# Optimization experiments

Measured on AMD Instinct MI355X. Metric: run time of the kernel, lower is better.

The kernel has to match this reference:

```python
import jax, jax.numpy as jnp
import numpy as np

D_MODEL = 1024
N_HEADS = 16
D_HEAD = D_MODEL // N_HEADS
D_FF = 4096
BATCH = 2
SEQ = 2048
LN_EPS = 1e-5


def setup_inputs() -> dict:
    key = jax.random.key(0)
    ks = jax.random.split(key, 12)
    s = 1.0 / np.sqrt(D_MODEL)
    x = jax.random.normal(ks[0], (BATCH, SEQ, D_MODEL), dtype=jnp.float32)
    mask = jnp.broadcast_to(jnp.tril(jnp.ones((SEQ, SEQ), jnp.int32)), (BATCH, SEQ, SEQ))
    return {
        "x": x,
        "mask": mask,
        # per-head projections stacked: [H, D, Dh] (bias=False in source)
        "Wq": jax.random.normal(ks[1], (N_HEADS, D_MODEL, D_HEAD), jnp.float32) * s,
        "Wk": jax.random.normal(ks[2], (N_HEADS, D_MODEL, D_HEAD), jnp.float32) * s,
        "Wv": jax.random.normal(ks[3], (N_HEADS, D_MODEL, D_HEAD), jnp.float32) * s,
        "Wo": jax.random.normal(ks[4], (D_MODEL, D_MODEL), jnp.float32) * s,
        "ln1_w": jnp.ones((D_MODEL,), jnp.float32),
        "ln1_b": jnp.zeros((D_MODEL,), jnp.float32),
        "ln2_w": jnp.ones((D_MODEL,), jnp.float32),
        "ln2_b": jnp.zeros((D_MODEL,), jnp.float32),
        "W1": jax.random.normal(ks[5], (D_MODEL, D_FF), jnp.float32) * s,
        "b1": jnp.zeros((D_FF,), jnp.float32),
        "W2": jax.random.normal(ks[6], (D_FF, D_MODEL), jnp.float32) * (1.0 / np.sqrt(D_FF)),
        "b2": jnp.zeros((D_MODEL,), jnp.float32),
    }


def layer_norm(x, w, b):
    mu = jnp.mean(x, axis=-1, keepdims=True)
    var = jnp.var(x, axis=-1, keepdims=True)
    return (x - mu) * jax.lax.rsqrt(var + LN_EPS) * w + b


def reference(x, mask, Wq, Wk, Wv, Wo, ln1_w, ln1_b, ln2_w, ln2_b, W1, b1, W2, b2):
    # pre-LN masked self-attention
    h = layer_norm(x, ln1_w, ln1_b)
    q = jnp.einsum("bsd,hde->bhse", h, Wq)  # [B,H,S,Dh]
    k = jnp.einsum("bsd,hde->bhse", h, Wk)
    v = jnp.einsum("bsd,hde->bhse", h, Wv)
    scores = jnp.einsum("bhse,bhte->bhst", q, k) / np.sqrt(D_HEAD)
    scores = jnp.where(mask[:, None, :, :].astype(bool), scores, -jnp.inf)
    weights = jax.nn.softmax(scores, axis=-1)
    attn = jnp.einsum("bhst,bhte->bhse", weights, v)  # [B,H,S,Dh]
    # concat heads (head order = last-dim order in torch.cat)
    concat = attn.transpose(0, 2, 1, 3).reshape(x.shape[0], x.shape[1], D_MODEL)
    att_out = concat @ Wo
    att_x = x + att_out
    # FFN with exact (erf) GELU, matching nn.GELU default
    h2 = layer_norm(att_x, ln2_w, ln2_b)
    ff = jax.nn.gelu(h2 @ W1 + b1, approximate=False) @ W2 + b2
    return att_x + ff
```

## Files before the change

kernel.cpp:

```cpp
#include <hip/hip_runtime.h>
#include <hip/hip_bf16.h>
#include <math.h>

#define D_MODEL 1024
#define N_HEADS 16
#define D_HEAD  64
#define D_FF    4096
#define BATCH   2
#define SEQ     2048
#define NTOK    (BATCH*SEQ)

typedef __hip_bfloat16 bf16;
typedef __attribute__((ext_vector_type(8))) short short8;
typedef __attribute__((ext_vector_type(4))) float floatx4;

template<typename TIN>
__global__ void ln_kernel(const TIN* __restrict__ x,
                          const float* __restrict__ w,
                          const float* __restrict__ b,
                          bf16* __restrict__ out) {
    int row = blockIdx.x;
    int tid = threadIdx.x;
    const long base = (long)row * D_MODEL;
    float v[4];
    float s = 0.f, sq = 0.f;
#pragma unroll
    for (int i = 0; i < 4; ++i) {
        float xv = (float)x[base + tid + i*256];
        v[i] = xv; s += xv; sq += xv*xv;
    }
    __shared__ float r1[256], r2[256];
    r1[tid] = s; r2[tid] = sq; __syncthreads();
    for (int off = 128; off > 0; off >>= 1) {
        if (tid < off) { r1[tid] += r1[tid+off]; r2[tid] += r2[tid+off]; }
        __syncthreads();
    }
    float mean = r1[0] * (1.f/D_MODEL);
    float var  = r2[0] * (1.f/D_MODEL) - mean*mean;
    float rstd = rsqrtf(var + 1e-5f);
#pragma unroll
    for (int i = 0; i < 4; ++i) {
        int c = tid + i*256;
        out[base + c] = __float2bfloat16((v[i] - mean) * rstd * w[c] + b[c]);
    }
}

__global__ __launch_bounds__(256) void wcvt_kernel(const float* __restrict__ W,
                                                   bf16* __restrict__ Wt,
                                                   int K, int N) {
    __shared__ float t[32][33];
    int n0 = blockIdx.x * 32, k0 = blockIdx.y * 32;
    int lx = threadIdx.x & 31, ly = threadIdx.x >> 5;
#pragma unroll
    for (int i = 0; i < 4; ++i) {
        int k = ly + i * 8;
        t[k][lx] = W[(long)(k0 + k) * N + n0 + lx];
    }
    __syncthreads();
#pragma unroll
    for (int i = 0; i < 4; ++i) {
        int n = ly + i * 8;
        Wt[(long)(n0 + n) * K + k0 + lx] = __float2bfloat16(t[lx][n]);
    }
}

__global__ __launch_bounds__(256) void wcvt_wo_w1(const float* __restrict__ Wo,
                                                  const float* __restrict__ W1,
                                                  bf16* __restrict__ wo_bf,
                                                  bf16* __restrict__ w1_bf) {
    __shared__ float t[32][33];
    int gx = blockIdx.x;
    const float* W; bf16* Wt; int N, n0;
    if (gx < 32) { W = Wo; Wt = wo_bf; N = D_MODEL; n0 = gx * 32; }
    else         { W = W1; Wt = w1_bf; N = D_FF;    n0 = (gx - 32) * 32; }
    int k0 = blockIdx.y * 32;
    int lx = threadIdx.x & 31, ly = threadIdx.x >> 5;
#pragma unroll
    for (int i = 0; i < 4; ++i) {
        int k = ly + i * 8;
        t[k][lx] = W[(long)(k0 + k) * N + n0 + lx];
    }
    __syncthreads();
#pragma unroll
    for (int i = 0; i < 4; ++i) {
        int n = ly + i * 8;
        Wt[(long)(n0 + n) * D_MODEL + k0 + lx] = __float2bfloat16(t[lx][n]);
    }
}

__global__ __launch_bounds__(256) void wcvt_qkv(const float* __restrict__ Wq,
                                                const float* __restrict__ Wk,
                                                const float* __restrict__ Wv,
                                                bf16* __restrict__ outp) {
    __shared__ float t[32][33];
    int z = blockIdx.z, mat = z >> 4, head = z & 15;
    const float* W = (mat == 0 ? Wq : mat == 1 ? Wk : Wv) + (long)head * D_MODEL * D_HEAD;
    bf16* Wt = outp + (long)z * D_HEAD * D_MODEL;
    int n0 = blockIdx.x * 32, k0 = blockIdx.y * 32;
    int lx = threadIdx.x & 31, ly = threadIdx.x >> 5;
#pragma unroll
    for (int i = 0; i < 4; ++i) {
        int k = ly + i * 8;
        t[k][lx] = W[(long)(k0 + k) * D_HEAD + n0 + lx];
    }
    __syncthreads();
#pragma unroll
    for (int i = 0; i < 4; ++i) {
        int n = ly + i * 8;
        Wt[(long)(n0 + n) * D_MODEL + k0 + lx] = __float2bfloat16(t[lx][n]);
    }
}

__device__ inline void swz2d(int& bx, int& by) {
    int gx = gridDim.x;
    int nwg = gx * gridDim.y;
    int bid = blockIdx.y * gx + blockIdx.x;
    int swz = (bid & 7) * (nwg >> 3) + (bid >> 3);
    bx = swz % gx;
    by = swz / gx;
}

template<int ROWS>
__device__ inline void stage_tile(const bf16* g, int gstride, short* lds) {
    int lane = threadIdx.x & 63, wave = threadIdx.x >> 6;
#pragma unroll
    for (int it = 0; it < ROWS / 64; ++it) {
        int c = wave + it * 4;
        const bf16* gp = g + (long)(c * 16 + (lane >> 2)) * gstride + (lane & 3) * 8;
        short* lp = lds + c * 512 + lane * 8;
        __builtin_amdgcn_global_load_lds(
            (const __attribute__((address_space(1))) void*)gp,
            (__attribute__((address_space(3))) void*)lp, 16, 0, 0);
    }
}

template<int BM, int BN, int BK>
__device__ inline void gemm_accum(const bf16* __restrict__ A, int lda,
                                  const bf16* __restrict__ Wt, int K,
                                  int row0, int col0, short* As, short* Bs,
                                  floatx4 (&acc)[BM/32][BN/32]) {
    constexpr int MI  = BM / 32;
    constexpr int NR  = BN / 32;
    constexpr int ASZ = BM * BK;
    constexpr int BSZ = BN * BK;
    int tid  = threadIdx.x;
    int wave = tid >> 6, lane = tid & 63;
    int quad = lane >> 4, l16 = lane & 15;
    int wm = (wave >> 1) * (BM / 2);
    int wn = (wave & 1) * (BN / 2);

    auto stage = [&](int k0, int buf) {
#pragma unroll
        for (int kk = 0; kk < BK; kk += 32) {
            stage_tile<BM>(A  + (long)row0 * lda + k0 + kk, lda,
                           As + buf * ASZ + (kk / 32) * BM * 32);
            stage_tile<BN>(Wt + (long)col0 * K   + k0 + kk, K,
                           Bs + buf * BSZ + (kk / 32) * BN * 32);
        }
    };

    stage(0, 0);
    __syncthreads();

    int cur = 0;
    for (int k0 = 0; k0 < K; k0 += BK) {
        if (k0 + BK < K) stage(k0 + BK, cur ^ 1);

#pragma unroll
        for (int p = 0; p < BK / 32; ++p) {
            const short* Ap = As + cur * ASZ + p * BM * 32;
            const short* Bp = Bs + cur * BSZ + p * BN * 32;
            short8 af[MI], bfr[NR];
#pragma unroll
            for (int mi = 0; mi < MI; ++mi)
                af[mi] = *(const short8*)&Ap[(wm + mi * 16 + l16) * 32 + quad * 8];
#pragma unroll
            for (int ni = 0; ni < NR; ++ni)
                bfr[ni] = *(const short8*)&Bp[(wn + ni * 16 + l16) * 32 + quad * 8];
#pragma unroll
            for (int mi = 0; mi < MI; ++mi)
#pragma unroll
                for (int ni = 0; ni < NR; ++ni)
                    acc[mi][ni] = __builtin_amdgcn_mfma_f32_16x16x32_bf16(
                        af[mi], bfr[ni], acc[mi][ni], 0, 0, 0);
        }
        __syncthreads();
        cur ^= 1;
    }
}

template<int BM, int BN, int BK, int BIAS, int ACT, int RES, int OUTBF16>
__global__ __launch_bounds__(256) void mfma_gemm_bf(
    const bf16* __restrict__ A, int lda,
    const bf16* __restrict__ Wt, int K,
    const float* __restrict__ bias, const float* __restrict__ resid,
    void* __restrict__ Cout, int ldc)
{
    constexpr int MI = BM / 32;
    constexpr int NR = BN / 32;
    __shared__ short As[2 * BM * BK];
    __shared__ short Bs[2 * BN * BK];
    int bx, by; swz2d(bx, by);
    int row0 = by * BM, col0 = bx * BN;
    int tid = threadIdx.x, wave = tid >> 6, lane = tid & 63;
    int quad = lane >> 4, l16 = lane & 15;
    int wm = (wave >> 1) * (BM / 2);
    int wn = (wave & 1) * (BN / 2);

    floatx4 acc[MI][NR];
#pragma unroll
    for (int mi = 0; mi < MI; ++mi)
#pragma unroll
        for (int ni = 0; ni < NR; ++ni)
            acc[mi][ni] = (floatx4){0.f, 0.f, 0.f, 0.f};

    gemm_accum<BM, BN, BK>(A, lda, Wt, K, row0, col0, As, Bs, acc);

#pragma unroll
    for (int mi = 0; mi < MI; ++mi) {
#pragma unroll
        for (int ni = 0; ni < NR; ++ni) {
#pragma unroll
            for (int r = 0; r < 4; ++r) {
                int row = row0 + wm + mi * 16 + quad * 4 + r;
                int col = col0 + wn + ni * 16 + l16;
                float v = acc[mi][ni][r];
                if (BIAS) v += bias[col];
                if (ACT == 1) {
                    float x2 = v * v;
                    float arg = fminf(v * fmaf(0.1029392f, x2, 2.3021182f), 20.f);
                    float t = exp2f(arg);
                    v = v * t * __builtin_amdgcn_rcpf(t + 1.f);
                }
                long idx = (long)row * ldc + col;
                if (RES == 1) v += resid[idx];
                if (OUTBF16) ((bf16*)Cout)[idx] = __float2bfloat16(v);
                else         ((float*)Cout)[idx] = v;
            }
        }
    }
}

struct QkvOut { bf16* o[3]; };
__global__ __launch_bounds__(256) void qkv_kernel(const bf16* __restrict__ h1,
                                                  const bf16* __restrict__ wqkv,
                                                  QkvOut a) {
    __shared__ short As[2 * 128 * 32];
    __shared__ short Bs[2 * 128 * 32];
    int bx, by; swz2d(bx, by);
    int row0 = by * 128, col0 = bx * 128;
    int tid = threadIdx.x, wave = tid >> 6, lane = tid & 63;
    int quad = lane >> 4, l16 = lane & 15;
    int wm = (wave >> 1) * 64, wn = (wave & 1) * 64;

    floatx4 acc[4][4];
#pragma unroll
    for (int mi = 0; mi < 4; ++mi)
#pragma unroll
        for (int ni = 0; ni < 4; ++ni)
            acc[mi][ni] = (floatx4){0.f, 0.f, 0.f, 0.f};

    gemm_accum<128, 128, 32>(h1, D_MODEL, wqkv, D_MODEL, row0, col0, As, Bs, acc);

#pragma unroll
    for (int mi = 0; mi < 4; ++mi) {
#pragma unroll
        for (int ni = 0; ni < 4; ++ni) {
#pragma unroll
            for (int r = 0; r < 4; ++r) {
                int row = row0 + wm + mi * 16 + quad * 4 + r;
                int c   = col0 + wn + ni * 16 + l16;
                int mat = c >> 10, hd = (c >> 6) & 15, d = c & 63;
                int b = row >> 11, s = row & 2047;
                a.o[mat][(((long)(b * 16 + hd) * SEQ + s) << 6) + d] =
                    __float2bfloat16(acc[mi][ni][r]);
            }
        }
    }
}

__global__ __launch_bounds__(256) void fattn_mfma(const bf16* __restrict__ q,
                                                  const bf16* __restrict__ k,
                                                  const bf16* __restrict__ v,
                                                  bf16* __restrict__ po,
                                                  float* __restrict__ lz) {
    int byr = blockIdx.y;
    int tile = (byr < 8) ? byr : 23 - byr;
    int chunk = blockIdx.z;
    int bh = blockIdx.x;
    int tid = threadIdx.x;
    int wave = tid >> 6, lane = tid & 63;
    int quad = lane >> 4, l16 = lane & 15;
    const long base = (long)bh * SEQ * D_HEAD;
    const int r0g = tile * 128;

    bf16*  pob = po + (long)chunk * 32 * SEQ * 64;
    float* lzb = lz + (long)chunk * 32 * SEQ;

    __shared__ short Ks[64 * 72];
    __shared__ short Vt[64 * 72];
    __shared__ short Ps[4][32 * 72];

    short8 qf[2][2];
#pragma unroll
    for (int rb = 0; rb < 2; ++rb) {
        const short* qrow = (const short*)(q + base +
            (long)(r0g + wave * 32 + rb * 16 + l16) * D_HEAD);
        qf[rb][0] = *(const short8*)(qrow + quad * 8);
        qf[rb][1] = *(const short8*)(qrow + 32 + quad * 8);
#pragma unroll
        for (int c = 0; c < 2; ++c)
#pragma unroll
            for (int j = 0; j < 8; ++j) {
                float f = __uint_as_float(((unsigned)(unsigned short)qf[rb][c][j]) << 16)
                          * 0.18033688f;
                qf[rb][c][j] = __builtin_bit_cast(short, __float2bfloat16(f));
            }
    }

    short8 onesf;
    {
        short o1 = (l16 == 0) ? (short)0x3F80 : (short)0;
#pragma unroll
        for (int j = 0; j < 8; ++j) onesf[j] = o1;
    }

    floatx4 o[2][4];
#pragma unroll
    for (int rb = 0; rb < 2; ++rb)
#pragma unroll
        for (int nb = 0; nb < 4; ++nb) o[rb][nb] = (floatx4){0.f, 0.f, 0.f, 0.f};
    floatx4 l4[2] = {(floatx4){0.f,0.f,0.f,0.f}, (floatx4){0.f,0.f,0.f,0.f}};

    const int kt0 = chunk ? tile + 1 : 0;
    const int kt1 = chunk ? 2 * tile + 1 : tile;
    for (int kt = kt0; kt <= kt1; ++kt) {
        __syncthreads();
        {
            int t = tid >> 2, c = tid & 3;
            const short* krow = (const short*)(k + base + (long)(kt * 64 + t) * D_HEAD);
            *(uint4*)&Ks[t * 72 + c * 16]     = *(const uint4*)(krow + c * 16);
            *(uint4*)&Ks[t * 72 + c * 16 + 8] = *(const uint4*)(krow + c * 16 + 8);
        }
        {
            int tp = (tid & 31) * 2;
            int d0 = ((tid >> 5) & 7) * 8;
            const short* v0 = (const short*)(v + base + (long)(kt * 64 + tp) * D_HEAD + d0);
            short va[8], vb[8];
            *(uint4*)va = *(const uint4*)v0;
            *(uint4*)vb = *(const uint4*)(v0 + D_HEAD);
#pragma unroll
            for (int j = 0; j < 8; ++j) {
                unsigned pk = (unsigned)(unsigned short)va[j] |
                              ((unsigned)(unsigned short)vb[j] << 16);
                *(unsigned*)&Vt[(d0 + j) * 72 + tp] = pk;
            }
        }
        __syncthreads();

        if (kt * 64 > r0g + wave * 32 + 31) continue;

        floatx4 s[2][4];
#pragma unroll
        for (int nb = 0; nb < 4; ++nb) {
            short8 kf0 = *(const short8*)&Ks[(nb * 16 + l16) * 72 + quad * 8];
            short8 kf1 = *(const short8*)&Ks[(nb * 16 + l16) * 72 + 32 + quad * 8];
#pragma unroll
            for (int rb = 0; rb < 2; ++rb) {
                floatx4 z4 = (floatx4){0.f, 0.f, 0.f, 0.f};
                z4 = __builtin_amdgcn_mfma_f32_16x16x32_bf16(qf[rb][0], kf0, z4, 0, 0, 0);
                z4 = __builtin_amdgcn_mfma_f32_16x16x32_bf16(qf[rb][1], kf1, z4, 0, 0, 0);
                s[rb][nb] = z4;
            }
        }

        if (kt >= 2 * tile) {
#pragma unroll
            for (int rb = 0; rb < 2; ++rb) {
                int qg = r0g + wave * 32 + rb * 16 + quad * 4;
#pragma unroll
                for (int nb = 0; nb < 4; ++nb) {
                    int kg = kt * 64 + nb * 16 + l16;
#pragma unroll
                    for (int r = 0; r < 4; ++r)
                        if (kg > qg + r) s[rb][nb][r] = -1e30f;
                }
            }
        }

        short* Pw = &Ps[wave][0];
#pragma unroll
        for (int rb = 0; rb < 2; ++rb)
#pragma unroll
            for (int nb = 0; nb < 4; ++nb)
#pragma unroll
                for (int r = 0; r < 4; ++r) {
                    float p = exp2f(s[rb][nb][r]);
                    Pw[(rb * 16 + quad * 4 + r) * 72 + nb * 16 + l16] =
                        __builtin_bit_cast(short, __float2bfloat16(p));
                }

        short8 pf[2][2];
#pragma unroll
        for (int rb = 0; rb < 2; ++rb) {
            pf[rb][0] = *(const short8*)&Pw[(rb * 16 + l16) * 72 + quad * 8];
            pf[rb][1] = *(const short8*)&Pw[(rb * 16 + l16) * 72 + 32 + quad * 8];
        }
#pragma unroll
        for (int nb = 0; nb < 4; ++nb) {
            short8 vf0 = *(const short8*)&Vt[(nb * 16 + l16) * 72 + quad * 8];
            short8 vf1 = *(const short8*)&Vt[(nb * 16 + l16) * 72 + 32 + quad * 8];
#pragma unroll
            for (int rb = 0; rb < 2; ++rb) {
                o[rb][nb] = __builtin_amdgcn_mfma_f32_16x16x32_bf16(pf[rb][0], vf0, o[rb][nb], 0, 0, 0);
                o[rb][nb] = __builtin_amdgcn_mfma_f32_16x16x32_bf16(pf[rb][1], vf1, o[rb][nb], 0, 0, 0);
            }
        }
#pragma unroll
        for (int rb = 0; rb < 2; ++rb) {
            l4[rb] = __builtin_amdgcn_mfma_f32_16x16x32_bf16(pf[rb][0], onesf, l4[rb], 0, 0, 0);
            l4[rb] = __builtin_amdgcn_mfma_f32_16x16x32_bf16(pf[rb][1], onesf, l4[rb], 0, 0, 0);
        }
    }

#pragma unroll
    for (int rb = 0; rb < 2; ++rb) {
#pragma unroll
        for (int nb = 0; nb < 4; ++nb)
#pragma unroll
            for (int r = 0; r < 4; ++r) {
                int row = r0g + wave * 32 + rb * 16 + quad * 4 + r;
                pob[((long)bh * SEQ + row) * 64 + nb * 16 + l16] =
                    __float2bfloat16(o[rb][nb][r]);
            }
        if (l16 == 0) {
#pragma unroll
            for (int r = 0; r < 4; ++r) {
                int row = r0g + wave * 32 + rb * 16 + quad * 4 + r;
                lzb[(long)bh * SEQ + row] = l4[rb][r];
            }
        }
    }
}

__global__ __launch_bounds__(256) void attn_combine(const bf16* __restrict__ po,
                                                    const float* __restrict__ lz,
                                                    bf16* __restrict__ cc) {
    const long CH = 32L * SEQ * 64;
    int row = blockIdx.x;
    int b = row >> 11, s = row & 2047;
    int tid = threadIdx.x;
    int col = tid * 4;
    int h = col >> 6, d = col & 63;
    long pidx = ((long)(b * 16 + h) * SEQ + s) * 64 + d;
    uint2 u0 = *(const uint2*)((const unsigned short*)po + pidx);
    uint2 u1 = *(const uint2*)((const unsigned short*)po + CH + pidx);
    long li = (long)(b * 16 + h) * SEQ + s;
    float linv = 1.f / (lz[li] + lz[32L * SEQ + li]);
    unsigned ua[4] = {u0.x & 0xFFFFu, u0.x >> 16, u0.y & 0xFFFFu, u0.y >> 16};
    unsigned ub[4] = {u1.x & 0xFFFFu, u1.x >> 16, u1.y & 0xFFFFu, u1.y >> 16};
    unsigned short rr[4];
#pragma unroll
    for (int i = 0; i < 4; ++i) {
        float ov = __uint_as_float(ua[i] << 16) + __uint_as_float(ub[i] << 16);
        rr[i] = __builtin_bit_cast(unsigned short, __float2bfloat16(ov * linv));
    }
    uint2 w;
    w.x = (unsigned)rr[0] | ((unsigned)rr[1] << 16);
    w.y = (unsigned)rr[2] | ((unsigned)rr[3] << 16);
    *(uint2*)((unsigned short*)cc + (long)row * D_MODEL + col) = w;
}

extern "C" void kernel_launch(void* const* d_in, const int* in_sizes, int n_in,
                              void* d_out, int out_size, void* d_ws, size_t ws_size,
                              hipStream_t stream) {
    const float* x    = (const float*)d_in[0];
    const float* Wq   = (const float*)d_in[2];
    const float* Wk   = (const float*)d_in[3];
    const float* Wv   = (const float*)d_in[4];
    const float* Wo   = (const float*)d_in[5];
    const float* ln1w = (const float*)d_in[6];
    const float* ln1b = (const float*)d_in[7];
    const float* ln2w = (const float*)d_in[8];
    const float* ln2b = (const float*)d_in[9];
    const float* W1   = (const float*)d_in[10];
    const float* b1   = (const float*)d_in[11];
    const float* W2   = (const float*)d_in[12];
    const float* b2   = (const float*)d_in[13];
    float* out = (float*)d_out;

    char* wsb = (char*)d_ws;
    const size_t MB = 1024*1024;
    bf16*  h1      = (bf16*)(wsb + 0*MB);
    bf16*  qb      = (bf16*)(wsb + 8*MB);
    bf16*  kb      = (bf16*)(wsb + 16*MB);
    bf16*  vb      = (bf16*)(wsb + 24*MB);
    bf16*  wqkv_bf = (bf16*)(wsb + 32*MB);
    bf16*  po      = (bf16*)(wsb + 32*MB);
    float* lz      = (float*)(wsb + 48*MB);
    bf16*  cc      = (bf16*)(wsb + 0*MB);
    bf16*  wo_bf   = (bf16*)(wsb + 8*MB);
    bf16*  w1_bf   = (bf16*)(wsb + 10*MB);
    bf16*  h2      = (bf16*)(wsb + 0*MB);
    bf16*  ff      = (bf16*)(wsb + 24*MB);
    bf16*  w2_bf   = (bf16*)(wsb + 8*MB);

    ln_kernel<float><<<NTOK, 256, 0, stream>>>(x, ln1w, ln1b, h1);

    wcvt_qkv<<<dim3(2, 32, 48), 256, 0, stream>>>(Wq, Wk, Wv, wqkv_bf);

    QkvOut qa; qa.o[0] = qb; qa.o[1] = kb; qa.o[2] = vb;
    qkv_kernel<<<dim3(24, 32), 256, 0, stream>>>(h1, wqkv_bf, qa);

    fattn_mfma<<<dim3(BATCH*N_HEADS, SEQ/128, 2), 256, 0, stream>>>(qb, kb, vb, po, lz);

    attn_combine<<<NTOK, 256, 0, stream>>>(po, lz, cc);

    wcvt_wo_w1<<<dim3(160, 32), 256, 0, stream>>>(Wo, W1, wo_bf, w1_bf);

    mfma_gemm_bf<64,128,64,0,0,1,0><<<dim3(8,64), 256, 0, stream>>>(
        cc, D_MODEL, wo_bf, D_MODEL, nullptr, x, out, D_MODEL);

    ln_kernel<float><<<NTOK, 256, 0, stream>>>(out, ln2w, ln2b, h2);

    mfma_gemm_bf<128,128,32,1,1,0,1><<<dim3(32,32), 256, 0, stream>>>(
        h2, D_MODEL, w1_bf, D_MODEL, b1, nullptr, ff, D_FF);

    wcvt_kernel<<<dim3(D_MODEL/32, D_FF/32), 256, 0, stream>>>(W2, w2_bf, D_FF, D_MODEL);

    mfma_gemm_bf<64,128,64,1,0,1,0><<<dim3(8,64), 256, 0, stream>>>(
        ff, D_FF, w2_bf, D_FF, b2, out, out, D_MODEL);
}
```

Before: 381.9 us.

## Add 256x256 direct-to-LDS pipelined GEMM for QKV and FFN1

New measurement: 382.4 us. No clear change (+0.1%).

```diff
diff --git a/kernel.cpp b/kernel.cpp
--- a/kernel.cpp
+++ b/kernel.cpp
@@ -241,39 +241,179 @@
     }
 }
 
+
 struct QkvOut { bf16* o[3]; };
-__global__ __launch_bounds__(256) void qkv_kernel(const bf16* __restrict__ h1,
-                                                  const bf16* __restrict__ wqkv,
-                                                  QkvOut a) {
-    __shared__ short As[2 * 128 * 32];
-    __shared__ short Bs[2 * 128 * 32];
-    int bx, by; swz2d(bx, by);
-    int row0 = by * 128, col0 = bx * 128;
-    int tid = threadIdx.x, wave = tid >> 6, lane = tid & 63;
+
+#define RG(buf,mat,kh) (((buf)*4 + (mat)*2 + (kh)) * 8192)
+#define G256_BAR  asm volatile("s_barrier" ::: "memory")
+#define G256_VM4  asm volatile("s_waitcnt vmcnt(4)" ::: "memory")
+#define G256_VM0  asm volatile("s_waitcnt vmcnt(0)" ::: "memory")
+
+__device__ inline void stage2(const bf16* g0, const bf16* g1, int koff, short* lp) {
+    __builtin_amdgcn_global_load_lds(
+        (const __attribute__((address_space(1))) void*)(g0 + koff),
+        (__attribute__((address_space(3))) void*)lp, 16, 0, 0);
+    __builtin_amdgcn_global_load_lds(
+        (const __attribute__((address_space(1))) void*)(g1 + koff),
+        (__attribute__((address_space(3))) void*)(lp + 4096), 16, 0, 0);
+}
+
+template<int MH>
+__device__ inline void rd_frags(const short* lds, int ra, int rb,
+                                int wr, int wc, int l16, int quad,
+                                short8 (&areg)[4], short8 (&breg)[4]) {
+    if (MH == 0) {
+#pragma unroll
+        for (int ni = 0; ni < 4; ++ni) {
+            int row = wc * 64 + ni * 16 + l16;
+            int sl = quad ^ ((row >> 1) & 3);
+            breg[ni] = *(const short8*)&lds[rb + row * 32 + sl * 8];
+        }
+    }
+#pragma unroll
+    for (int mi = 0; mi < 4; ++mi) {
+        int row = wr * 128 + (MH * 4 + mi) * 16 + l16;
+        int sl = quad ^ ((row >> 1) & 3);
+        areg[mi] = *(const short8*)&lds[ra + row * 32 + sl * 8];
+    }
+}
+
+template<int MH>
+__device__ inline void do_mfma16(const short8 (&areg)[4], const short8 (&breg)[4],
+                                 floatx4 (&acc)[8][4]) {
+    __builtin_amdgcn_s_setprio(1);
+#pragma unroll
+    for (int mi = 0; mi < 4; ++mi)
+#pragma unroll
+        for (int ni = 0; ni < 4; ++ni)
+            acc[MH * 4 + mi][ni] = __builtin_amdgcn_mfma_f32_16x16x32_bf16(
+                areg[mi], breg[ni], acc[MH * 4 + mi][ni], 0, 0, 0);
+    __builtin_amdgcn_s_setprio(0);
+}
+
+template<int EPI>
+__global__ __launch_bounds__(512, 1) void gemm256_kernel(
+    const bf16* __restrict__ A, int lda,
+    const bf16* __restrict__ Wt, int K,
+    const float* __restrict__ bias,
+    bf16* __restrict__ Cout, int ldc, QkvOut qa)
+{
+    __shared__ short lds[65536];
+    const int NT = K / 64;
+    int row0 = blockIdx.y * 256, col0 = blockIdx.x * 256;
+    int tid = threadIdx.x;
+    int lane = tid & 63, wave = tid >> 6;
     int quad = lane >> 4, l16 = lane & 15;
-    int wm = (wave >> 1) * 64, wn = (wave & 1) * 64;
-
-    floatx4 acc[4][4];
-#pragma unroll
-    for (int mi = 0; mi < 4; ++mi)
+    int wr = wave >> 2, wc = wave & 3;
+
+    int srow = tid >> 2, slot = tid & 3;
+    int cA0 = slot ^ ((srow >> 1) & 3);
+    int cA1 = slot ^ (((srow + 128) >> 1) & 3);
+    const bf16* a0 = A  + (long)(row0 + srow) * lda + cA0 * 8;
+    const bf16* a1 = A  + (long)(row0 + srow + 128) * lda + cA1 * 8;
+    const bf16* b0 = Wt + (long)(col0 + srow) * K + cA0 * 8;
+    const bf16* b1 = Wt + (long)(col0 + srow + 128) * K + cA1 * 8;
+    short* lt = lds + tid * 8;
+
+    floatx4 acc[8][4];
+#pragma unroll
+    for (int mi = 0; mi < 8; ++mi)
 #pragma unroll
         for (int ni = 0; ni < 4; ++ni)
             acc[mi][ni] = (floatx4){0.f, 0.f, 0.f, 0.f};
 
-    gemm_accum<128, 128, 32>(h1, D_MODEL, wqkv, D_MODEL, row0, col0, As, Bs, acc);
-
-#pragma unroll
-    for (int mi = 0; mi < 4; ++mi) {
+    stage2(a0, a1, 0,  lt + RG(0,0,0));
+    stage2(b0, b1, 0,  lt + RG(0,1,0));
+    stage2(a0, a1, 32, lt + RG(0,0,1));
+    stage2(b0, b1, 32, lt + RG(0,1,1));
+    stage2(a0, a1, 64, lt + RG(1,0,0));
+    stage2(b0, b1, 64, lt + RG(1,1,0));
+    G256_VM4;
+    G256_BAR;
+
+    short8 areg[4], breg[4];
+
+    for (int i = 0; i < NT / 2; ++i) {
+        int T = 2 * i;
+        bool s2 = (T + 2 < NT);
+        bool s3 = (T + 3 < NT);
+        int k1off = (T + 1) * 64;
+        int k2off = (T + 2) * 64;
+        int k3off = (T + 3) * 64;
+
+        rd_frags<0>(lds, RG(0,0,0), RG(0,1,0), wr, wc, l16, quad, areg, breg);
+        stage2(a0, a1, k1off + 32, lt + RG(1,0,1));
+        G256_BAR;
+        do_mfma16<0>(areg, breg, acc);
+        G256_BAR;
+
+        rd_frags<1>(lds, RG(0,0,0), RG(0,1,0), wr, wc, l16, quad, areg, breg);
+        stage2(b0, b1, k1off + 32, lt + RG(1,1,1));
+        G256_BAR;
+        do_mfma16<1>(areg, breg, acc);
+        G256_BAR;
+
+        rd_frags<0>(lds, RG(0,0,1), RG(0,1,1), wr, wc, l16, quad, areg, breg);
+        if (s2) stage2(a0, a1, k2off, lt + RG(0,0,0));
+        G256_BAR;
+        do_mfma16<0>(areg, breg, acc);
+        G256_BAR;
+
+        rd_frags<1>(lds, RG(0,0,1), RG(0,1,1), wr, wc, l16, quad, areg, breg);
+        if (s2) stage2(b0, b1, k2off, lt + RG(0,1,0));
+        G256_BAR;
+        do_mfma16<1>(areg, breg, acc);
+        if (s2) { G256_VM4; } else { G256_VM0; }
+        G256_BAR;
+
+        rd_frags<0>(lds, RG(1,0,0), RG(1,1,0), wr, wc, l16, quad, areg, breg);
+        if (s2) stage2(a0, a1, k2off + 32, lt + RG(0,0,1));
+        G256_BAR;
+        do_mfma16<0>(areg, breg, acc);
+        G256_BAR;
+
+        rd_frags<1>(lds, RG(1,0,0), RG(1,1,0), wr, wc, l16, quad, areg, breg);
+        if (s2) stage2(b0, b1, k2off + 32, lt + RG(0,1,1));
+        G256_BAR;
+        do_mfma16<1>(areg, breg, acc);
+        G256_BAR;
+
+        rd_frags<0>(lds, RG(1,0,1), RG(1,1,1), wr, wc, l16, quad, areg, breg);
+        if (s3) stage2(a0, a1, k3off, lt + RG(1,0,0));
+        G256_BAR;
+        do_mfma16<0>(areg, breg, acc);
+        G256_BAR;
+
+        rd_frags<1>(lds, RG(1,0,1), RG(1,1,1), wr, wc, l16, quad, areg, breg);
+        if (s3) stage2(b0, b1, k3off, lt + RG(1,1,0));
+        G256_BAR;
+        do_mfma16<1>(areg, breg, acc);
+        if (s3) { G256_VM4; } else { G256_VM0; }
+        G256_BAR;
+    }
+
+#pragma unroll
+    for (int mi = 0; mi < 8; ++mi) {
 #pragma unroll
         for (int ni = 0; ni < 4; ++ni) {
 #pragma unroll
             for (int r = 0; r < 4; ++r) {
-                int row = row0 + wm + mi * 16 + quad * 4 + r;
-                int c   = col0 + wn + ni * 16 + l16;
-                int mat = c >> 10, hd = (c >> 6) & 15, d = c & 63;
-                int b = row >> 11, s = row & 2047;
-                a.o[mat][(((long)(b * 16 + hd) * SEQ + s) << 6) + d] =
-                    __float2bfloat16(acc[mi][ni][r]);
+                int row = row0 + wr * 128 + mi * 16 + quad * 4 + r;
+                int col = col0 + wc * 64 + ni * 16 + l16;
+                float v = acc[mi][ni][r];
+                if constexpr (EPI == 0) {
+                    v += bias[col];
+                    float x2 = v * v;
+                    float arg = fminf(v * fmaf(0.1029392f, x2, 2.3021182f), 20.f);
+                    float t = exp2f(arg);
+                    v = v * t * __builtin_amdgcn_rcpf(t + 1.f);
+                    Cout[(long)row * ldc + col] = __float2bfloat16(v);
+                } else {
+                    int mat = col >> 10, hd = (col >> 6) & 15, d = col & 63;
+                    int b = row >> 11, s = row & 2047;
+                    qa.o[mat][(((long)(b * 16 + hd) * SEQ + s) << 6) + d] =
+                        __float2bfloat16(v);
+                }
             }
         }
     }
@@ -505,12 +645,15 @@
     bf16*  ff      = (bf16*)(wsb + 24*MB);
     bf16*  w2_bf   = (bf16*)(wsb + 8*MB);
 
+    QkvOut qa; qa.o[0] = qb; qa.o[1] = kb; qa.o[2] = vb;
+    QkvOut qdummy = {};
+
     ln_kernel<float><<<NTOK, 256, 0, stream>>>(x, ln1w, ln1b, h1);
 
     wcvt_qkv<<<dim3(2, 32, 48), 256, 0, stream>>>(Wq, Wk, Wv, wqkv_bf);
 
-    QkvOut qa; qa.o[0] = qb; qa.o[1] = kb; qa.o[2] = vb;
-    qkv_kernel<<<dim3(24, 32), 256, 0, stream>>>(h1, wqkv_bf, qa);
+    gemm256_kernel<1><<<dim3(12, 16), 512, 0, stream>>>(
+        h1, D_MODEL, wqkv_bf, D_MODEL, nullptr, nullptr, 0, qa);
 
     fattn_mfma<<<dim3(BATCH*N_HEADS, SEQ/128, 2), 256, 0, stream>>>(qb, kb, vb, po, lz);
 
@@ -523,8 +666,8 @@
 
     ln_kernel<float><<<NTOK, 256, 0, stream>>>(out, ln2w, ln2b, h2);
 
-    mfma_gemm_bf<128,128,32,1,1,0,1><<<dim3(32,32), 256, 0, stream>>>(
-        h2, D_MODEL, w1_bf, D_MODEL, b1, nullptr, ff, D_FF);
+    gemm256_kernel<0><<<dim3(16, 16), 512, 0, stream>>>(
+        h2, D_MODEL, w1_bf, D_MODEL, b1, ff, D_FF, qdummy);
 
     wcvt_kernel<<<dim3(D_MODEL/32, D_FF/32), 256, 0, stream>>>(W2, w2_bf, D_FF, D_MODEL);
 
```
